# Performance work log

Measured on AMD Instinct MI355X. Metric: run time of the kernel, lower is better.

## Reference

```python
import jax, jax.numpy as jnp
import numpy as np

B, V, FC, J = 1024, 5023, 9976, 5
NSHAPE, NEXP = 100, 50
PARENTS = np.array([-1, 0, 1, 1, 1])
NECK_CHAIN = np.array([1, 0])  # neck then its parent (global)


def batch_rodrigues(rv):
    # rv: [N,3] axis-angle -> [N,3,3] rotation matrices
    angle = jnp.linalg.norm(rv + 1e-8, axis=1, keepdims=True)  # [N,1]
    n = rv / angle
    rx, ry, rz = n[:, 0], n[:, 1], n[:, 2]
    z = jnp.zeros_like(rx)
    K = jnp.stack([z, -rz, ry, rz, z, -rx, -ry, rx, z], axis=1).reshape(-1, 3, 3)
    s = jnp.sin(angle)[..., None]
    c = jnp.cos(angle)[..., None]
    I = jnp.eye(3, dtype=rv.dtype)
    return I + s * K + (1.0 - c) * jnp.matmul(K, K)


def setup_inputs() -> dict:
    key = jax.random.key(0)
    ks = jax.random.split(key, 16)
    inp = {}
    inp["shape_params"] = jax.random.normal(ks[0], (B, NSHAPE), jnp.float32)
    inp["expression_params"] = jax.random.normal(ks[1], (B, NEXP), jnp.float32)
    inp["pose_params"] = jax.random.normal(ks[2], (B, 6), jnp.float32) * 0.2
    inp["v_template"] = jax.random.normal(ks[3], (V, 3), jnp.float32) * 0.1
    inp["shapedirs"] = jax.random.normal(ks[4], (V, 3, NSHAPE + NEXP), jnp.float32) * 0.01
    inp["posedirs"] = jax.random.normal(ks[5], (36, V * 3), jnp.float32) * 0.01
    Jr = jax.random.uniform(ks[6], (J, V), jnp.float32)
    inp["J_regressor"] = Jr / Jr.sum(1, keepdims=True)
    Wl = jax.random.uniform(ks[7], (V, J), jnp.float32)
    inp["lbs_weights"] = Wl / Wl.sum(1, keepdims=True)
    inp["neck_pose"] = jnp.zeros((1, 3), jnp.float32)
    inp["eye_pose"] = jnp.zeros((1, 6), jnp.float32)
    inp["faces"] = jax.random.randint(ks[8], (FC, 3), 0, V)
    inp["lmk_faces_idx"] = jax.random.randint(ks[9], (51,), 0, FC)
    b = jax.random.uniform(ks[10], (51, 3), jnp.float32)
    inp["lmk_bary_coords"] = b / b.sum(-1, keepdims=True)
    inp["dynamic_lmk_faces_idx"] = jax.random.randint(ks[11], (79, 17), 0, FC)
    db = jax.random.uniform(ks[12], (79, 17, 3), jnp.float32)
    inp["dynamic_lmk_bary_coords"] = db / db.sum(-1, keepdims=True)
    inp["full_lmk_faces_idx"] = jax.random.randint(ks[13], (68,), 0, FC)
    fb = jax.random.uniform(ks[14], (68, 3), jnp.float32)
    inp["full_lmk_bary_coords"] = fb / fb.sum(-1, keepdims=True)
    return inp


def reference(shape_params, expression_params, pose_params, v_template, shapedirs,
              posedirs, J_regressor, lbs_weights, neck_pose, eye_pose, faces,
              lmk_faces_idx, lmk_bary_coords, dynamic_lmk_faces_idx,
              dynamic_lmk_bary_coords, full_lmk_faces_idx, full_lmk_bary_coords):
    b = shape_params.shape[0]
    dt = shape_params.dtype
    betas = jnp.concatenate([shape_params, expression_params], 1)  # [B,150]
    full_pose = jnp.concatenate([pose_params[:, :3],
                                 jnp.broadcast_to(neck_pose, (b, 3)),
                                 pose_params[:, 3:],
                                 jnp.broadcast_to(eye_pose, (b, 6))], 1)  # [B,15]
    # shape/expression blendshapes
    v_shaped = v_template[None] + jnp.einsum('bl,vcl->bvc', betas, shapedirs)  # [B,V,3]
    joints = jnp.einsum('jv,bvc->bjc', J_regressor, v_shaped)  # [B,J,3]
    rot_mats = batch_rodrigues(full_pose.reshape(-1, 3)).reshape(b, J, 3, 3)
    ident = jnp.eye(3, dtype=dt)
    pose_feature = (rot_mats[:, 1:] - ident).reshape(b, -1)  # [B,36]
    v_posed = v_shaped + (pose_feature @ posedirs).reshape(b, V, 3)
    # kinematic chain of rigid transforms
    rel_joints = joints.at[:, 1:].add(-joints[:, PARENTS[1:]])
    tmat = jnp.concatenate([rot_mats, rel_joints[..., None]], -1)  # [B,J,3,4]
    bottom = jnp.broadcast_to(jnp.array([0., 0., 0., 1.], dt), (b, J, 1, 4))
    tmat = jnp.concatenate([tmat, bottom], 2)  # [B,J,4,4]
    chains = [tmat[:, 0]]
    for i in range(1, J):
        chains.append(chains[PARENTS[i]] @ tmat[:, i])
    transforms = jnp.stack(chains, 1)  # [B,J,4,4]
    joints_h = jnp.concatenate([joints, jnp.zeros((b, J, 1), dt)], -1)
    rel_tf = transforms - jnp.pad(transforms @ joints_h[..., None],
                                  ((0, 0), (0, 0), (0, 0), (3, 0)))
    # linear blend skinning
    T = jnp.einsum('vj,bjmn->bvmn', lbs_weights, rel_tf)  # [B,V,4,4]
    v_h = jnp.concatenate([v_posed, jnp.ones((b, V, 1), dt)], -1)
    vertices = jnp.einsum('bvmn,bvn->bvm', T, v_h)[..., :3]  # [B,V,3]
    # dynamic contour landmark selection via neck kinematic chain yaw
    aa = full_pose.reshape(b, J, 3)[:, NECK_CHAIN]  # [B,2,3]
    rch = batch_rodrigues(aa.reshape(-1, 3)).reshape(b, 2, 3, 3)
    rel_rot = rch[:, 1] @ rch[:, 0]  # loop order: R_global @ R_neck
    sy = jnp.sqrt(rel_rot[:, 0, 0] ** 2 + rel_rot[:, 1, 0] ** 2)
    yang = jnp.arctan2(-rel_rot[:, 2, 0], sy) * (180.0 / np.pi)
    y = jnp.round(jnp.minimum(yang, 39.0)).astype(jnp.int32)
    neg = y < 0
    big = y < -39
    y = jnp.where(neg, jnp.where(big, 78, 39 - y), y)
    dyn_faces = dynamic_lmk_faces_idx[y]   # [B,17]
    dyn_bary = dynamic_lmk_bary_coords[y]  # [B,17,3]
    lf = jnp.concatenate([dyn_faces,
                          jnp.broadcast_to(lmk_faces_idx[None], (b,) + lmk_faces_idx.shape)], 1)
    lb = jnp.concatenate([dyn_bary,
                          jnp.broadcast_to(lmk_bary_coords[None], (b,) + lmk_bary_coords.shape)], 1)

    def _lmk(verts, lfaces, lbary):
        tri = faces[lfaces]  # [B,L,3] vertex ids
        lv = jax.vmap(lambda v, t: v[t])(verts, tri)  # [B,L,3,3]
        return jnp.einsum('blfc,blf->blc', lv, lbary)

    landmarks2d = _lmk(vertices, lf, lb)  # [B,68,3]
    full_lf = jnp.broadcast_to(full_lmk_faces_idx[None], (b,) + full_lmk_faces_idx.shape)
    full_lb = jnp.broadcast_to(full_lmk_bary_coords[None], (b,) + full_lmk_bary_coords.shape)
    landmarks3d = _lmk(vertices, full_lf, full_lb)  # [B,68,3]
    return vertices, landmarks2d, landmarks3d
```

## Files before the change

kernel.cpp:

```cpp
#include <hip/hip_runtime.h>
#include <math.h>

#define BATCH 1024
#define NV 5023
#define NJ 5
#define K1 150
#define K2 36
#define KTOT 186
#define MCOLS (NV*3)
#define NCHUNK 80
#define CHUNKV 63

typedef __attribute__((ext_vector_type(4))) float floatx4;

#define WS_JSD     0
#define WS_RELTF   2272
#define WS_Y       63712
#define WS_AT      64736
#define WS_PARTIAL 64736

__device__ __forceinline__ void rodrigues(const float* rv, float* R) {
  const float ex = rv[0]+1e-8f, ey = rv[1]+1e-8f, ez = rv[2]+1e-8f;
  const float angle = sqrtf(ex*ex + ey*ey + ez*ez);
  const float inv = 1.0f/angle;
  const float nx = rv[0]*inv, ny = rv[1]*inv, nz = rv[2]*inv;
  const float s = sinf(angle), c = cosf(angle);
  const float omc = 1.0f - c;
  R[0] = 1.0f - omc*(ny*ny+nz*nz);
  R[1] = -s*nz + omc*nx*ny;
  R[2] =  s*ny + omc*nx*nz;
  R[3] =  s*nz + omc*nx*ny;
  R[4] = 1.0f - omc*(nx*nx+nz*nz);
  R[5] = -s*nx + omc*ny*nz;
  R[6] = -s*ny + omc*nx*nz;
  R[7] =  s*nx + omc*ny*nz;
  R[8] = 1.0f - omc*(nx*nx+ny*ny);
}

__launch_bounds__(512)
__global__ void k1_jsd_partial(const float* __restrict__ jreg, const float* __restrict__ shdirs,
                               const float* __restrict__ vtemp, float* __restrict__ partial) {
  const int chunk = blockIdx.x;
  const int t = threadIdx.x;
  if (t >= 453) return;
  const int v0 = chunk*CHUNKV;
  const int v1 = (v0 + CHUNKV < NV) ? v0 + CHUNKV : NV;
  float acc[5] = {0.f,0.f,0.f,0.f,0.f};
  if (t < 450) {
    for (int v = v0; v < v1; ++v) {
      const float sv = shdirs[(size_t)v*450 + t];
      #pragma unroll
      for (int j=0;j<5;++j) acc[j] = fmaf(jreg[j*NV + v], sv, acc[j]);
    }
  } else {
    const int c = t - 450;
    for (int v = v0; v < v1; ++v) {
      const float sv = vtemp[v*3 + c];
      #pragma unroll
      for (int j=0;j<5;++j) acc[j] = fmaf(jreg[j*NV + v], sv, acc[j]);
    }
  }
  #pragma unroll
  for (int j=0;j<5;++j)
    partial[(size_t)(chunk*NJ + j)*453 + t] = acc[j];
}

__launch_bounds__(256)
__global__ void k1b_jsd_reduce(const float* __restrict__ partial, float* __restrict__ jsd) {
  const int i = blockIdx.x*256 + threadIdx.x;
  if (i >= NJ*453) return;
  float s = 0.0f;
  for (int c = 0; c < NCHUNK; ++c) s += partial[(size_t)c*(NJ*453) + i];
  jsd[i] = s;
}

__launch_bounds__(256)
__global__ void k2_pose(const float* __restrict__ shape, const float* __restrict__ expr,
                        const float* __restrict__ pose, const float* __restrict__ neck,
                        const float* __restrict__ eye, const float* __restrict__ jsd,
                        float* __restrict__ At, float* __restrict__ reltf,
                        int* __restrict__ yidx) {
  const int b = blockIdx.x*256 + threadIdx.x;
  if (b >= BATCH) return;

  float fp[15];
  fp[0]=pose[b*6+0]; fp[1]=pose[b*6+1]; fp[2]=pose[b*6+2];
  fp[3]=neck[0];     fp[4]=neck[1];     fp[5]=neck[2];
  fp[6]=pose[b*6+3]; fp[7]=pose[b*6+4]; fp[8]=pose[b*6+5];
  #pragma unroll
  for (int i=0;i<6;++i) fp[9+i] = eye[i];

  float R[5][9];
  #pragma unroll
  for (int j=0;j<5;++j) rodrigues(&fp[j*3], R[j]);

  for (int l=0;l<100;++l) At[(size_t)l*BATCH + b] = shape[(size_t)b*100 + l];
  for (int l=0;l<50;++l)  At[(size_t)(100+l)*BATCH + b] = expr[(size_t)b*50 + l];
  #pragma unroll
  for (int jj=0;jj<4;++jj)
    #pragma unroll
    for (int rc=0;rc<9;++rc)
      At[(size_t)(K1 + jj*9 + rc)*BATCH + b] = R[1+jj][rc] - ((rc==0||rc==4||rc==8)?1.0f:0.0f);

  float jac[15];
  #pragma unroll
  for (int jc=0;jc<15;++jc) jac[jc] = jsd[(jc/3)*453 + 450 + (jc%3)];
  for (int l=0;l<150;++l) {
    const float bv = (l<100) ? shape[(size_t)b*100+l] : expr[(size_t)b*50 + (l-100)];
    #pragma unroll
    for (int jc=0;jc<15;++jc)
      jac[jc] = fmaf(jsd[(jc/3)*453 + (jc%3)*150 + l], bv, jac[jc]);
  }

  float C[5][12];
  #pragma unroll
  for (int r=0;r<3;++r) {
    C[0][r*4+0]=R[0][r*3+0]; C[0][r*4+1]=R[0][r*3+1]; C[0][r*4+2]=R[0][r*3+2];
    C[0][r*4+3]=jac[r];
  }
  const int par[5] = {-1,0,1,1,1};
  #pragma unroll
  for (int i=1;i<5;++i) {
    const int p = par[i];
    const float rj0 = jac[i*3+0]-jac[p*3+0];
    const float rj1 = jac[i*3+1]-jac[p*3+1];
    const float rj2 = jac[i*3+2]-jac[p*3+2];
    #pragma unroll
    for (int r=0;r<3;++r) {
      const float c0=C[p][r*4+0], c1=C[p][r*4+1], c2=C[p][r*4+2], c3=C[p][r*4+3];
      C[i][r*4+0] = c0*R[i][0] + c1*R[i][3] + c2*R[i][6];
      C[i][r*4+1] = c0*R[i][1] + c1*R[i][4] + c2*R[i][7];
      C[i][r*4+2] = c0*R[i][2] + c1*R[i][5] + c2*R[i][8];
      C[i][r*4+3] = c0*rj0 + c1*rj1 + c2*rj2 + c3;
    }
  }

  float* rt = reltf + (size_t)b*60;
  #pragma unroll
  for (int j=0;j<5;++j) {
    const float jx=jac[j*3+0], jy=jac[j*3+1], jz=jac[j*3+2];
    #pragma unroll
    for (int r=0;r<3;++r) {
      const float m0=C[j][r*4+0], m1=C[j][r*4+1], m2=C[j][r*4+2], m3=C[j][r*4+3];
      rt[j*12+r*4+0]=m0; rt[j*12+r*4+1]=m1; rt[j*12+r*4+2]=m2;
      rt[j*12+r*4+3]=m3 - (m0*jx + m1*jy + m2*jz);
    }
  }

  const float c00=R[1][0], c10=R[1][3], c20=R[1][6];
  const float r00 = R[0][0]*c00 + R[0][1]*c10 + R[0][2]*c20;
  const float r10 = R[0][3]*c00 + R[0][4]*c10 + R[0][5]*c20;
  const float r20 = R[0][6]*c00 + R[0][7]*c10 + R[0][8]*c20;
  const float sy = sqrtf(r00*r00 + r10*r10);
  const float yang = atan2f(-r20, sy) * 57.29577951308232f;
  int y = (int)rintf(fminf(yang, 39.0f));
  if (y < 0) y = (y < -39) ? 78 : (39 - y);
  yidx[b] = y;
}

#define SROW 260

template<int KL, bool POSE>
__device__ __forceinline__ void chunk_body(int k0, int t, int vl, int aoff, int m0,
    const float* __restrict__ At, const float* __restrict__ shdirs,
    const float* __restrict__ pdirs, float* shB, float (&acc)[32][3]) {
  __syncthreads();
  if (!POSE) {
    constexpr int Q = KL/2;
    constexpr int TOT = 192*Q;
    for (int i = t; i < TOT; i += 256) {
      const int q  = i % Q;
      const int ml = i / Q;
      const int v  = ml/3, c = ml - v*3;
      int m = m0 + ml; if (m > MCOLS-1) m = MCOLS-1;
      const float2 f = *reinterpret_cast<const float2*>(shdirs + (size_t)m*K1 + k0 + 2*q);
      shB[(2*q)*SROW + v*4 + c]   = f.x;
      shB[(2*q+1)*SROW + v*4 + c] = f.y;
    }
  } else {
    constexpr int TOT = 192*KL;
    for (int i = t; i < TOT; i += 256) {
      const int kk = i / 192;
      const int ml = i - kk*192;
      const int v  = ml/3, c = ml - v*3;
      int m = m0 + ml; if (m > MCOLS-1) m = MCOLS-1;
      shB[kk*SROW + v*4 + c] = pdirs[(size_t)(k0 - K1 + kk)*MCOLS + m];
    }
  }
  __syncthreads();
  #pragma unroll 2
  for (int kk = 0; kk < KL; ++kk) {
    const float* ap = At + (size_t)(k0+kk)*BATCH + aoff;
    const floatx4 bv = *reinterpret_cast<const floatx4*>(shB + kk*SROW + vl*4);
    #pragma unroll
    for (int i=0;i<32;++i) {
      const float ai = ap[i];
      acc[i][0] = fmaf(ai, bv[0], acc[i][0]);
      acc[i][1] = fmaf(ai, bv[1], acc[i][1]);
      acc[i][2] = fmaf(ai, bv[2], acc[i][2]);
    }
  }
}

__launch_bounds__(256, 4)
__global__ void k3_valu(const float* __restrict__ At, const float* __restrict__ shdirs,
                        const float* __restrict__ pdirs, const float* __restrict__ vtemp,
                        const float* __restrict__ lbsw, const float* __restrict__ reltf,
                        float* __restrict__ vout) {
  __shared__ float shB[32*SROW];

  const int t  = threadIdx.x;
  const int vl = t & 63;
  const int bg = t >> 6;
  const int v0 = blockIdx.x * 64;
  const int b0 = blockIdx.y * 128;
  const int m0 = v0*3;
  const int aoff = __builtin_amdgcn_readfirstlane(b0 + bg*32);

  float acc[32][3] = {};

  #pragma unroll 1
  for (int ch = 0; ch < 4; ++ch)
    chunk_body<32,false>(ch*32, t, vl, aoff, m0, At, shdirs, pdirs, shB, acc);
  chunk_body<22,false>(128, t, vl, aoff, m0, At, shdirs, pdirs, shB, acc);
  chunk_body<32,true >(150, t, vl, aoff, m0, At, shdirs, pdirs, shB, acc);
  chunk_body<4, true >(182, t, vl, aoff, m0, At, shdirs, pdirs, shB, acc);

  const int v = v0 + vl;
  if (v < NV) {
    float w5[5];
    #pragma unroll
    for (int j=0;j<5;++j) w5[j] = lbsw[(size_t)v*5 + j];
    const float tx = vtemp[(size_t)v*3+0];
    const float ty = vtemp[(size_t)v*3+1];
    const float tz = vtemp[(size_t)v*3+2];
    #pragma unroll
    for (int i=0;i<32;++i) {
      const float* rl = reltf + (size_t)(aoff + i)*60;
      const float vx = acc[i][0]+tx, vy = acc[i][1]+ty, vz = acc[i][2]+tz;
      float o[3];
      #pragma unroll
      for (int r=0;r<3;++r) {
        float a0=0.f,a1=0.f,a2=0.f,a3=0.f;
        #pragma unroll
        for (int j=0;j<5;++j) {
          a0 = fmaf(w5[j], rl[j*12+r*4+0], a0);
          a1 = fmaf(w5[j], rl[j*12+r*4+1], a1);
          a2 = fmaf(w5[j], rl[j*12+r*4+2], a2);
          a3 = fmaf(w5[j], rl[j*12+r*4+3], a3);
        }
        o[r] = fmaf(a0, vx, fmaf(a1, vy, fmaf(a2, vz, a3)));
      }
      float* dst = vout + ((size_t)(aoff + i)*NV + v)*3;
      dst[0]=o[0]; dst[1]=o[1]; dst[2]=o[2];
    }
  }
}

__launch_bounds__(192)
__global__ void k4_landmarks(const float* __restrict__ verts, const int* __restrict__ faces,
                             const int* __restrict__ lmkf, const float* __restrict__ lmkb,
                             const int* __restrict__ dynf, const float* __restrict__ dynb,
                             const int* __restrict__ fullf, const float* __restrict__ fullb,
                             const int* __restrict__ yidx, float* __restrict__ out2d,
                             float* __restrict__ out3d) {
  const int b = blockIdx.x;
  const int t = threadIdx.x;
  if (t >= 136) return;
  const int which = t >= 68;
  const int i = which ? (t-68) : t;
  int fidx; float bw0,bw1,bw2;
  if (!which) {
    if (i < 17) {
      const int y = yidx[b];
      fidx = dynf[y*17 + i];
      const float* p = dynb + ((size_t)y*17 + i)*3;
      bw0=p[0]; bw1=p[1]; bw2=p[2];
    } else {
      fidx = lmkf[i-17];
      const float* p = lmkb + (size_t)(i-17)*3;
      bw0=p[0]; bw1=p[1]; bw2=p[2];
    }
  } else {
    fidx = fullf[i];
    const float* p = fullb + (size_t)i*3;
    bw0=p[0]; bw1=p[1]; bw2=p[2];
  }
  const int t0 = faces[fidx*3+0], t1 = faces[fidx*3+1], t2 = faces[fidx*3+2];
  const float* vb = verts + (size_t)b*NV*3;
  float* dst = (which ? out3d : out2d) + ((size_t)b*68 + i)*3;
  #pragma unroll
  for (int c=0;c<3;++c)
    dst[c] = vb[(size_t)t0*3+c]*bw0 + vb[(size_t)t1*3+c]*bw1 + vb[(size_t)t2*3+c]*bw2;
}

extern "C" void kernel_launch(void* const* d_in, const int* in_sizes, int n_in,
                              void* d_out, int out_size, void* d_ws, size_t ws_size,
                              hipStream_t stream) {
  const float* shape = (const float*)d_in[0];
  const float* expr  = (const float*)d_in[1];
  const float* pose  = (const float*)d_in[2];
  const float* vtemp = (const float*)d_in[3];
  const float* shdirs= (const float*)d_in[4];
  const float* pdirs = (const float*)d_in[5];
  const float* jreg  = (const float*)d_in[6];
  const float* lbsw  = (const float*)d_in[7];
  const float* neck  = (const float*)d_in[8];
  const float* eye   = (const float*)d_in[9];
  const int*   faces = (const int*)d_in[10];
  const int*   lmkf  = (const int*)d_in[11];
  const float* lmkb  = (const float*)d_in[12];
  const int*   dynf  = (const int*)d_in[13];
  const float* dynb  = (const float*)d_in[14];
  const int*   fullf = (const int*)d_in[15];
  const float* fullb = (const float*)d_in[16];

  float* wsf = (float*)d_ws;
  float* jsd     = wsf + WS_JSD;
  float* reltf   = wsf + WS_RELTF;
  int*   yidx    = (int*)(wsf + WS_Y);
  float* At      = wsf + WS_AT;
  float* partial = wsf + WS_PARTIAL;

  float* vout  = (float*)d_out;
  float* out2d = vout + (size_t)BATCH*NV*3;
  float* out3d = out2d + (size_t)BATCH*68*3;

  hipLaunchKernelGGL(k1_jsd_partial, dim3(NCHUNK), dim3(512), 0, stream,
                     jreg, shdirs, vtemp, partial);
  hipLaunchKernelGGL(k1b_jsd_reduce, dim3(9), dim3(256), 0, stream, partial, jsd);
  hipLaunchKernelGGL(k2_pose, dim3(4), dim3(256), 0, stream,
                     shape, expr, pose, neck, eye, jsd, At, reltf, yidx);
  hipLaunchKernelGGL(k3_valu, dim3(80, BATCH/128), dim3(256), 0, stream,
                     At, shdirs, pdirs, vtemp, lbsw, reltf, vout);
  hipLaunchKernelGGL(k4_landmarks, dim3(BATCH), dim3(192), 0, stream,
                     vout, faces, lmkf, lmkb, dynf, dynb, fullf, fullb, yidx, out2d, out3d);
}
```

Before: 184.1 us.

## Double-buffer shared-memory staging of blend-shape directions with smaller chunks

Splits the main GEMM-like loop into separate staging and compute phases over two 16-row shared buffers, so the next chunk's global loads are issued before the current chunk's FMAs, with one barrier per step instead of two. It also fully unrolls the inner k loop and prefetches the next shared-memory vector, and vectorizes the shape/expression loads in the per-batch joint computation. The intent is to hide global load latency behind arithmetic. In exchange it raises register pressure from the full unroll and prefetch, which could hurt occupancy at four blocks per SM.

After: 294.3 us. 1.6x slower.

```diff
diff --git a/kernel.cpp b/kernel.cpp
--- a/kernel.cpp
+++ b/kernel.cpp
@@ -105,11 +105,31 @@
   float jac[15];
   #pragma unroll
   for (int jc=0;jc<15;++jc) jac[jc] = jsd[(jc/3)*453 + 450 + (jc%3)];
-  for (int l=0;l<150;++l) {
-    const float bv = (l<100) ? shape[(size_t)b*100+l] : expr[(size_t)b*50 + (l-100)];
-    #pragma unroll
-    for (int jc=0;jc<15;++jc)
-      jac[jc] = fmaf(jsd[(jc/3)*453 + (jc%3)*150 + l], bv, jac[jc]);
+  {
+    const floatx4* sh4 = reinterpret_cast<const floatx4*>(shape + (size_t)b*100);
+    for (int l4=0; l4<25; ++l4) {
+      const floatx4 s4 = sh4[l4];
+      #pragma unroll
+      for (int u=0;u<4;++u) {
+        const int l = l4*4 + u;
+        const float bv = s4[u];
+        #pragma unroll
+        for (int jc=0;jc<15;++jc)
+          jac[jc] = fmaf(jsd[(jc/3)*453 + (jc%3)*150 + l], bv, jac[jc]);
+      }
+    }
+    const float2* ex2 = reinterpret_cast<const float2*>(expr + (size_t)b*50);
+    for (int l2=0; l2<25; ++l2) {
+      const float2 e2 = ex2[l2];
+      #pragma unroll
+      for (int u=0;u<2;++u) {
+        const int l = 100 + l2*2 + u;
+        const float bv = (u==0) ? e2.x : e2.y;
+        #pragma unroll
+        for (int jc=0;jc<15;++jc)
+          jac[jc] = fmaf(jsd[(jc/3)*453 + (jc%3)*150 + l], bv, jac[jc]);
+      }
+    }
   }
 
   float C[5][12];
@@ -159,12 +179,11 @@
 }
 
 #define SROW 260
+#define SCROWS 16
 
 template<int KL, bool POSE>
-__device__ __forceinline__ void chunk_body(int k0, int t, int vl, int aoff, int m0,
-    const float* __restrict__ At, const float* __restrict__ shdirs,
-    const float* __restrict__ pdirs, float* shB, float (&acc)[32][3]) {
-  __syncthreads();
+__device__ __forceinline__ void stage_chunk(int k0, int t, int m0,
+    const float* __restrict__ shdirs, const float* __restrict__ pdirs, float* shB) {
   if (!POSE) {
     constexpr int Q = KL/2;
     constexpr int TOT = 192*Q;
@@ -187,11 +206,18 @@
       shB[kk*SROW + v*4 + c] = pdirs[(size_t)(k0 - K1 + kk)*MCOLS + m];
     }
   }
-  __syncthreads();
-  #pragma unroll 2
+}
+
+template<int KL>
+__device__ __forceinline__ void compute_chunk(int k0, int vl, int aoff,
+    const float* __restrict__ At, const float* shB, float (&acc)[32][3]) {
+  const float* base = shB + vl*4;
+  floatx4 bv = *reinterpret_cast<const floatx4*>(base);
+  #pragma unroll
   for (int kk = 0; kk < KL; ++kk) {
+    floatx4 bvn = bv;
+    if (kk + 1 < KL) bvn = *reinterpret_cast<const floatx4*>(base + (kk+1)*SROW);
     const float* ap = At + (size_t)(k0+kk)*BATCH + aoff;
-    const floatx4 bv = *reinterpret_cast<const floatx4*>(shB + kk*SROW + vl*4);
     #pragma unroll
     for (int i=0;i<32;++i) {
       const float ai = ap[i];
@@ -199,6 +225,7 @@
       acc[i][1] = fmaf(ai, bv[1], acc[i][1]);
       acc[i][2] = fmaf(ai, bv[2], acc[i][2]);
     }
+    bv = bvn;
   }
 }
 
@@ -207,7 +234,7 @@
                         const float* __restrict__ pdirs, const float* __restrict__ vtemp,
                         const float* __restrict__ lbsw, const float* __restrict__ reltf,
                         float* __restrict__ vout) {
-  __shared__ float shB[32*SROW];
+  __shared__ float shB[2*SCROWS*SROW];
 
   const int t  = threadIdx.x;
   const int vl = t & 63;
@@ -216,15 +243,50 @@
   const int b0 = blockIdx.y * 128;
   const int m0 = v0*3;
   const int aoff = __builtin_amdgcn_readfirstlane(b0 + bg*32);
+  float* B0 = shB;
+  float* B1 = shB + SCROWS*SROW;
 
   float acc[32][3] = {};
 
-  #pragma unroll 1
-  for (int ch = 0; ch < 4; ++ch)
-    chunk_body<32,false>(ch*32, t, vl, aoff, m0, At, shdirs, pdirs, shB, acc);
-  chunk_body<22,false>(128, t, vl, aoff, m0, At, shdirs, pdirs, shB, acc);
-  chunk_body<32,true >(150, t, vl, aoff, m0, At, shdirs, pdirs, shB, acc);
-  chunk_body<4, true >(182, t, vl, aoff, m0, At, shdirs, pdirs, shB, acc);
+  stage_chunk<16,false>(  0, t, m0, shdirs, pdirs, B0);
+  __syncthreads();
+  stage_chunk<16,false>( 16, t, m0, shdirs, pdirs, B1);
+  compute_chunk<16>(  0, vl, aoff, At, B0, acc);
+  __syncthreads();
+  stage_chunk<16,false>( 32, t, m0, shdirs, pdirs, B0);
+  compute_chunk<16>( 16, vl, aoff, At, B1, acc);
+  __syncthreads();
+  stage_chunk<16,false>( 48, t, m0, shdirs, pdirs, B1);
+  compute_chunk<16>( 32, vl, aoff, At, B0, acc);
+  __syncthreads();
+  stage_chunk<16,false>( 64, t, m0, shdirs, pdirs, B0);
+  compute_chunk<16>( 48, vl, aoff, At, B1, acc);
+  __syncthreads();
+  stage_chunk<16,false>( 80, t, m0, shdirs, pdirs, B1);
+  compute_chunk<16>( 64, vl, aoff, At, B0, acc);
+  __syncthreads();
+  stage_chunk<16,false>( 96, t, m0, shdirs, pdirs, B0);
+  compute_chunk<16>( 80, vl, aoff, At, B1, acc);
+  __syncthreads();
+  stage_chunk<16,false>(112, t, m0, shdirs, pdirs, B1);
+  compute_chunk<16>( 96, vl, aoff, At, B0, acc);
+  __syncthreads();
+  stage_chunk<16,false>(128, t, m0, shdirs, pdirs, B0);
+  compute_chunk<16>(112, vl, aoff, At, B1, acc);
+  __syncthreads();
+  stage_chunk<6, false>(144, t, m0, shdirs, pdirs, B1);
+  compute_chunk<16>(128, vl, aoff, At, B0, acc);
+  __syncthreads();
+  stage_chunk<16,true >(150, t, m0, shdirs, pdirs, B0);
+  compute_chunk<6>(144, vl, aoff, At, B1, acc);
+  __syncthreads();
+  stage_chunk<16,true >(166, t, m0, shdirs, pdirs, B1);
+  compute_chunk<16>(150, vl, aoff, At, B0, acc);
+  __syncthreads();
+  stage_chunk<4, true >(182, t, m0, shdirs, pdirs, B0);
+  compute_chunk<16>(166, vl, aoff, At, B1, acc);
+  __syncthreads();
+  compute_chunk<4>(182, vl, aoff, At, B0, acc);
 
   const int v = v0 + vl;
   if (v < NV) {
```

## Double-buffer shared-memory K chunks with register prefetch in vertex GEMM

Applied to the files above, without the earlier changes.

Replaces the single 32-row shared buffer with two 8-row buffers and a register-staged prefetch, so the global loads for the next K chunk are issued before computing the current one and written to the other buffer afterward. This targets global load latency that was previously exposed between the synchronisations around each chunk. It also vectorises the shape/expression reads in the joint regression loop. The trade-off is more barriers, since chunks are smaller, and extra registers for the prefetch on top of the 96-float accumulator.

Measured after the change: 215.4 us. 17.0% more time.

```diff
diff --git a/kernel.cpp b/kernel.cpp
--- a/kernel.cpp
+++ b/kernel.cpp
@@ -105,11 +105,31 @@
   float jac[15];
   #pragma unroll
   for (int jc=0;jc<15;++jc) jac[jc] = jsd[(jc/3)*453 + 450 + (jc%3)];
-  for (int l=0;l<150;++l) {
-    const float bv = (l<100) ? shape[(size_t)b*100+l] : expr[(size_t)b*50 + (l-100)];
-    #pragma unroll
-    for (int jc=0;jc<15;++jc)
-      jac[jc] = fmaf(jsd[(jc/3)*453 + (jc%3)*150 + l], bv, jac[jc]);
+  {
+    const floatx4* sh4 = reinterpret_cast<const floatx4*>(shape + (size_t)b*100);
+    for (int l4=0; l4<25; ++l4) {
+      const floatx4 s4 = sh4[l4];
+      #pragma unroll
+      for (int u=0;u<4;++u) {
+        const int l = l4*4 + u;
+        const float bv = s4[u];
+        #pragma unroll
+        for (int jc=0;jc<15;++jc)
+          jac[jc] = fmaf(jsd[(jc/3)*453 + (jc%3)*150 + l], bv, jac[jc]);
+      }
+    }
+    const float2* ex2 = reinterpret_cast<const float2*>(expr + (size_t)b*50);
+    for (int l2=0; l2<25; ++l2) {
+      const float2 e2 = ex2[l2];
+      #pragma unroll
+      for (int u=0;u<2;++u) {
+        const int l = 100 + l2*2 + u;
+        const float bv = (u==0) ? e2.x : e2.y;
+        #pragma unroll
+        for (int jc=0;jc<15;++jc)
+          jac[jc] = fmaf(jsd[(jc/3)*453 + (jc%3)*150 + l], bv, jac[jc]);
+      }
+    }
   }
 
   float C[5][12];
@@ -159,35 +179,73 @@
 }
 
 #define SROW 260
-
-template<int KL, bool POSE>
-__device__ __forceinline__ void chunk_body(int k0, int t, int vl, int aoff, int m0,
-    const float* __restrict__ At, const float* __restrict__ shdirs,
-    const float* __restrict__ pdirs, float* shB, float (&acc)[32][3]) {
-  __syncthreads();
-  if (!POSE) {
-    constexpr int Q = KL/2;
-    constexpr int TOT = 192*Q;
-    for (int i = t; i < TOT; i += 256) {
-      const int q  = i % Q;
-      const int ml = i / Q;
-      const int v  = ml/3, c = ml - v*3;
+#define CR 8
+
+template<int KL>
+__device__ __forceinline__ void sload_shape(int k0, int t, int m0,
+    const float* __restrict__ shdirs, float2* r) {
+  constexpr int Q = KL/2;
+  constexpr int TOT = 192*Q;
+  constexpr int NIT = (TOT+255)/256;
+  #pragma unroll
+  for (int n=0;n<NIT;++n){
+    const int i = t + n*256;
+    if ((TOT%256==0) || (i<TOT)) {
+      const int q = i % Q, ml = i / Q;
       int m = m0 + ml; if (m > MCOLS-1) m = MCOLS-1;
-      const float2 f = *reinterpret_cast<const float2*>(shdirs + (size_t)m*K1 + k0 + 2*q);
-      shB[(2*q)*SROW + v*4 + c]   = f.x;
-      shB[(2*q+1)*SROW + v*4 + c] = f.y;
-    }
-  } else {
-    constexpr int TOT = 192*KL;
-    for (int i = t; i < TOT; i += 256) {
-      const int kk = i / 192;
-      const int ml = i - kk*192;
-      const int v  = ml/3, c = ml - v*3;
+      r[n] = *reinterpret_cast<const float2*>(shdirs + (size_t)m*K1 + k0 + 2*q);
+    }
+  }
+}
+template<int KL>
+__device__ __forceinline__ void swrite_shape(int t, const float2* r, float* buf) {
+  constexpr int Q = KL/2;
+  constexpr int TOT = 192*Q;
+  constexpr int NIT = (TOT+255)/256;
+  #pragma unroll
+  for (int n=0;n<NIT;++n){
+    const int i = t + n*256;
+    if ((TOT%256==0) || (i<TOT)) {
+      const int q = i % Q, ml = i / Q;
+      const int v = ml/3, c = ml - v*3;
+      buf[(2*q)*SROW + v*4 + c]   = r[n].x;
+      buf[(2*q+1)*SROW + v*4 + c] = r[n].y;
+    }
+  }
+}
+template<int KL>
+__device__ __forceinline__ void sload_pose(int k0, int t, int m0,
+    const float* __restrict__ pdirs, float* r) {
+  constexpr int TOT = 192*KL;
+  constexpr int NIT = (TOT+255)/256;
+  #pragma unroll
+  for (int n=0;n<NIT;++n){
+    const int i = t + n*256;
+    if ((TOT%256==0) || (i<TOT)) {
+      const int kk = i/192, ml = i - kk*192;
       int m = m0 + ml; if (m > MCOLS-1) m = MCOLS-1;
-      shB[kk*SROW + v*4 + c] = pdirs[(size_t)(k0 - K1 + kk)*MCOLS + m];
-    }
-  }
-  __syncthreads();
+      r[n] = pdirs[(size_t)(k0 - K1 + kk)*MCOLS + m];
+    }
+  }
+}
+template<int KL>
+__device__ __forceinline__ void swrite_pose(int t, const float* r, float* buf) {
+  constexpr int TOT = 192*KL;
+  constexpr int NIT = (TOT+255)/256;
+  #pragma unroll
+  for (int n=0;n<NIT;++n){
+    const int i = t + n*256;
+    if ((TOT%256==0) || (i<TOT)) {
+      const int kk = i/192, ml = i - kk*192;
+      const int v = ml/3, c = ml - v*3;
+      buf[kk*SROW + v*4 + c] = r[n];
+    }
+  }
+}
+
+template<int KL>
+__device__ __forceinline__ void compute_chunk(int k0, int vl, int aoff,
+    const float* __restrict__ At, const float* shB, float (&acc)[32][3]) {
   #pragma unroll 2
   for (int kk = 0; kk < KL; ++kk) {
     const float* ap = At + (size_t)(k0+kk)*BATCH + aoff;
@@ -207,7 +265,7 @@
                         const float* __restrict__ pdirs, const float* __restrict__ vtemp,
                         const float* __restrict__ lbsw, const float* __restrict__ reltf,
                         float* __restrict__ vout) {
-  __shared__ float shB[32*SROW];
+  __shared__ float shB[2*CR*SROW];
 
   const int t  = threadIdx.x;
   const int vl = t & 63;
@@ -216,15 +274,49 @@
   const int b0 = blockIdx.y * 128;
   const int m0 = v0*3;
   const int aoff = __builtin_amdgcn_readfirstlane(b0 + bg*32);
+  float* B0 = shB;
+  float* B1 = shB + CR*SROW;
 
   float acc[32][3] = {};
+  float2 rs[3];
+  float rp[6];
+
+  sload_shape<8>(0, t, m0, shdirs, rs);
+  swrite_shape<8>(t, rs, B0);
 
   #pragma unroll 1
-  for (int ch = 0; ch < 4; ++ch)
-    chunk_body<32,false>(ch*32, t, vl, aoff, m0, At, shdirs, pdirs, shB, acc);
-  chunk_body<22,false>(128, t, vl, aoff, m0, At, shdirs, pdirs, shB, acc);
-  chunk_body<32,true >(150, t, vl, aoff, m0, At, shdirs, pdirs, shB, acc);
-  chunk_body<4, true >(182, t, vl, aoff, m0, At, shdirs, pdirs, shB, acc);
+  for (int g=0; g<17; ++g) {
+    __syncthreads();
+    sload_shape<8>(8*(g+1), t, m0, shdirs, rs);
+    __builtin_amdgcn_sched_barrier(0);
+    compute_chunk<8>(8*g, vl, aoff, At, (g&1)?B1:B0, acc);
+    swrite_shape<8>(t, rs, (g&1)?B0:B1);
+  }
+  __syncthreads();
+  sload_shape<6>(144, t, m0, shdirs, rs);
+  __builtin_amdgcn_sched_barrier(0);
+  compute_chunk<8>(136, vl, aoff, At, B1, acc);
+  swrite_shape<6>(t, rs, B0);
+  __syncthreads();
+  sload_pose<8>(150, t, m0, pdirs, rp);
+  __builtin_amdgcn_sched_barrier(0);
+  compute_chunk<6>(144, vl, aoff, At, B0, acc);
+  swrite_pose<8>(t, rp, B1);
+  #pragma unroll 1
+  for (int g=19; g<22; ++g) {
+    __syncthreads();
+    sload_pose<8>(150 + 8*(g-18), t, m0, pdirs, rp);
+    __builtin_amdgcn_sched_barrier(0);
+    compute_chunk<8>(150 + 8*(g-19), vl, aoff, At, (g&1)?B1:B0, acc);
+    swrite_pose<8>(t, rp, (g&1)?B0:B1);
+  }
+  __syncthreads();
+  sload_pose<4>(182, t, m0, pdirs, rp);
+  __builtin_amdgcn_sched_barrier(0);
+  compute_chunk<8>(174, vl, aoff, At, B0, acc);
+  swrite_pose<4>(t, rp, B1);
+  __syncthreads();
+  compute_chunk<4>(182, vl, aoff, At, B1, acc);
 
   const int v = v0 + vl;
   if (v < NV) {
```

## Load blend-shape directions directly into registers instead of staging through LDS

Applied to the files above, without the earlier changes.

The main vertex GEMM kernel no longer stages shapedirs/posedirs tiles through shared memory with two barriers per chunk. Each thread now reads its own vertex's direction rows straight into registers in groups of 10 (shape) or 6 (pose) k-values. The launch-bounds occupancy hint drops from 4 to 3 to leave room for the extra registers. The joint-regressor loop in the setup kernel also uses vectorized loads of the shape and expression parameters. The trade-off is uncoalesced, strided global reads (rows 150 floats apart across lanes) and higher register pressure, in exchange for no LDS traffic and no block synchronization.

Result: slower. 217.7 us (+18.3%).

```diff
diff --git a/kernel.cpp b/kernel.cpp
--- a/kernel.cpp
+++ b/kernel.cpp
@@ -105,11 +105,31 @@
   float jac[15];
   #pragma unroll
   for (int jc=0;jc<15;++jc) jac[jc] = jsd[(jc/3)*453 + 450 + (jc%3)];
-  for (int l=0;l<150;++l) {
-    const float bv = (l<100) ? shape[(size_t)b*100+l] : expr[(size_t)b*50 + (l-100)];
-    #pragma unroll
-    for (int jc=0;jc<15;++jc)
-      jac[jc] = fmaf(jsd[(jc/3)*453 + (jc%3)*150 + l], bv, jac[jc]);
+  {
+    const floatx4* sh4 = reinterpret_cast<const floatx4*>(shape + (size_t)b*100);
+    for (int l4=0; l4<25; ++l4) {
+      const floatx4 s4 = sh4[l4];
+      #pragma unroll
+      for (int u=0;u<4;++u) {
+        const int l = l4*4 + u;
+        const float bv = s4[u];
+        #pragma unroll
+        for (int jc=0;jc<15;++jc)
+          jac[jc] = fmaf(jsd[(jc/3)*453 + (jc%3)*150 + l], bv, jac[jc]);
+      }
+    }
+    const float2* ex2 = reinterpret_cast<const float2*>(expr + (size_t)b*50);
+    for (int l2=0; l2<25; ++l2) {
+      const float2 e2 = ex2[l2];
+      #pragma unroll
+      for (int u=0;u<2;++u) {
+        const int l = 100 + l2*2 + u;
+        const float bv = (u==0) ? e2.x : e2.y;
+        #pragma unroll
+        for (int jc=0;jc<15;++jc)
+          jac[jc] = fmaf(jsd[(jc/3)*453 + (jc%3)*150 + l], bv, jac[jc]);
+      }
+    }
   }
 
   float C[5][12];
@@ -158,75 +178,73 @@
   yidx[b] = y;
 }
 
-#define SROW 260
-
-template<int KL, bool POSE>
-__device__ __forceinline__ void chunk_body(int k0, int t, int vl, int aoff, int m0,
-    const float* __restrict__ At, const float* __restrict__ shdirs,
-    const float* __restrict__ pdirs, float* shB, float (&acc)[32][3]) {
-  __syncthreads();
-  if (!POSE) {
-    constexpr int Q = KL/2;
-    constexpr int TOT = 192*Q;
-    for (int i = t; i < TOT; i += 256) {
-      const int q  = i % Q;
-      const int ml = i / Q;
-      const int v  = ml/3, c = ml - v*3;
-      int m = m0 + ml; if (m > MCOLS-1) m = MCOLS-1;
-      const float2 f = *reinterpret_cast<const float2*>(shdirs + (size_t)m*K1 + k0 + 2*q);
-      shB[(2*q)*SROW + v*4 + c]   = f.x;
-      shB[(2*q+1)*SROW + v*4 + c] = f.y;
-    }
-  } else {
-    constexpr int TOT = 192*KL;
-    for (int i = t; i < TOT; i += 256) {
-      const int kk = i / 192;
-      const int ml = i - kk*192;
-      const int v  = ml/3, c = ml - v*3;
-      int m = m0 + ml; if (m > MCOLS-1) m = MCOLS-1;
-      shB[kk*SROW + v*4 + c] = pdirs[(size_t)(k0 - K1 + kk)*MCOLS + m];
-    }
-  }
-  __syncthreads();
-  #pragma unroll 2
-  for (int kk = 0; kk < KL; ++kk) {
-    const float* ap = At + (size_t)(k0+kk)*BATCH + aoff;
-    const floatx4 bv = *reinterpret_cast<const floatx4*>(shB + kk*SROW + vl*4);
-    #pragma unroll
-    for (int i=0;i<32;++i) {
-      const float ai = ap[i];
-      acc[i][0] = fmaf(ai, bv[0], acc[i][0]);
-      acc[i][1] = fmaf(ai, bv[1], acc[i][1]);
-      acc[i][2] = fmaf(ai, bv[2], acc[i][2]);
-    }
-  }
-}
-
-__launch_bounds__(256, 4)
+__launch_bounds__(256, 3)
 __global__ void k3_valu(const float* __restrict__ At, const float* __restrict__ shdirs,
                         const float* __restrict__ pdirs, const float* __restrict__ vtemp,
                         const float* __restrict__ lbsw, const float* __restrict__ reltf,
                         float* __restrict__ vout) {
-  __shared__ float shB[32*SROW];
-
   const int t  = threadIdx.x;
   const int vl = t & 63;
   const int bg = t >> 6;
   const int v0 = blockIdx.x * 64;
   const int b0 = blockIdx.y * 128;
-  const int m0 = v0*3;
   const int aoff = __builtin_amdgcn_readfirstlane(b0 + bg*32);
 
+  const int v  = v0 + vl;
+  const int vc = (v < NV) ? v : NV-1;
+  const float* brow0 = shdirs + (size_t)(3*vc+0)*K1;
+  const float* brow1 = shdirs + (size_t)(3*vc+1)*K1;
+  const float* brow2 = shdirs + (size_t)(3*vc+2)*K1;
+
   float acc[32][3] = {};
 
   #pragma unroll 1
-  for (int ch = 0; ch < 4; ++ch)
-    chunk_body<32,false>(ch*32, t, vl, aoff, m0, At, shdirs, pdirs, shB, acc);
-  chunk_body<22,false>(128, t, vl, aoff, m0, At, shdirs, pdirs, shB, acc);
-  chunk_body<32,true >(150, t, vl, aoff, m0, At, shdirs, pdirs, shB, acc);
-  chunk_body<4, true >(182, t, vl, aoff, m0, At, shdirs, pdirs, shB, acc);
-
-  const int v = v0 + vl;
+  for (int g=0; g<15; ++g) {
+    const int k0 = g*10;
+    float ba[10], bb[10], bc[10];
+    #pragma unroll
+    for (int q=0;q<5;++q) {
+      const float2 f0 = *reinterpret_cast<const float2*>(brow0 + k0 + 2*q);
+      const float2 f1 = *reinterpret_cast<const float2*>(brow1 + k0 + 2*q);
+      const float2 f2 = *reinterpret_cast<const float2*>(brow2 + k0 + 2*q);
+      ba[2*q]=f0.x; ba[2*q+1]=f0.y;
+      bb[2*q]=f1.x; bb[2*q+1]=f1.y;
+      bc[2*q]=f2.x; bc[2*q+1]=f2.y;
+    }
+    #pragma unroll
+    for (int kk=0; kk<10; ++kk) {
+      const float* ap = At + (size_t)(k0+kk)*BATCH + aoff;
+      #pragma unroll
+      for (int i=0;i<32;++i) {
+        const float ai = ap[i];
+        acc[i][0] = fmaf(ai, ba[kk], acc[i][0]);
+        acc[i][1] = fmaf(ai, bb[kk], acc[i][1]);
+        acc[i][2] = fmaf(ai, bc[kk], acc[i][2]);
+      }
+    }
+  }
+  #pragma unroll 1
+  for (int g=0; g<6; ++g) {
+    const int kp0 = g*6;
+    float ba[6], bb[6], bc[6];
+    #pragma unroll
+    for (int kk=0;kk<6;++kk) {
+      const float* prow = pdirs + (size_t)(kp0+kk)*MCOLS + 3*vc;
+      ba[kk] = prow[0]; bb[kk] = prow[1]; bc[kk] = prow[2];
+    }
+    #pragma unroll
+    for (int kk=0; kk<6; ++kk) {
+      const float* ap = At + (size_t)(K1+kp0+kk)*BATCH + aoff;
+      #pragma unroll
+      for (int i=0;i<32;++i) {
+        const float ai = ap[i];
+        acc[i][0] = fmaf(ai, ba[kk], acc[i][0]);
+        acc[i][1] = fmaf(ai, bb[kk], acc[i][1]);
+        acc[i][2] = fmaf(ai, bc[kk], acc[i][2]);
+      }
+    }
+  }
+
   if (v < NV) {
     float w5[5];
     #pragma unroll
```
